# Performance work log

Measured on AMD Instinct MI355X. Metric: run time of the kernel, lower is better.

Reference implementation:

```python
import jax, jax.numpy as jnp
import numpy as np

B, S, E, D, H, L, V = 8, 128, 512, 1024, 16, 4, 32000
DH = D // H
FF = 4 * D
SCALE = 1.0 / (DH ** 0.5)
NEG = -1e30


def _layer_norm(x, g, b, eps=1e-5):
    m = jnp.mean(x, axis=-1, keepdims=True)
    v = jnp.mean((x - m) ** 2, axis=-1, keepdims=True)
    return (x - m) / jnp.sqrt(v + eps) * g + b


def _rel_shift(x):
    # x: [q, k, b, n] -> TransformerXL relative shift
    q, k, b, n = x.shape
    xp = jnp.concatenate([jnp.zeros((q, 1, b, n), x.dtype), x], axis=1)
    xp = xp.reshape(k + 1, q, b, n)
    return xp[1:].reshape(q, k, b, n)


def setup_inputs():
    key = jax.random.key(0)
    ks = jax.random.split(key, 40)
    g = lambda i, shape, s=0.02: jax.random.normal(ks[i], shape, jnp.float32) * s
    inp = {
        'input_ids': jax.random.randint(ks[0], (B, E), 0, V),
        'encoder_rep': jax.random.normal(ks[1], (B, E, D), jnp.float32),
        'input_mask': jnp.ones((B, E), jnp.float32),
        'decode_input': jax.random.randint(ks[2], (B, S), 0, V),
        'decode_target': jax.random.randint(ks[3], (B, S), 0, V),
        'word_emb': g(4, (V, D)),
        'qkv_w': g(5, (L, 3 * D, D)), 'r_w': g(6, (L, D, D)), 'o_w': g(7, (L, D, D)),
        'kv_w': g(8, (L, 2 * D, D)), 'q_w': g(9, (L, D, D)), 'io_w': g(10, (L, D, D)),
        'rr_bias': g(11, (L, H, DH)), 'rw_bias': g(12, (L, H, DH)),
        'ln1_g': jnp.ones((L, D)), 'ln1_b': jnp.zeros((L, D)),
        'ln2_g': jnp.ones((L, D)), 'ln2_b': jnp.zeros((L, D)),
        'ffn_w1': g(13, (L, FF, D)), 'ffn_b1': jnp.zeros((L, FF)),
        'ffn_w2': g(14, (L, D, FF)), 'ffn_b2': jnp.zeros((L, D)),
        'ln3_g': jnp.ones((L, D)), 'ln3_b': jnp.zeros((L, D)),
        'out_w': g(15, (D, D)), 'out_b': jnp.zeros((D,)),
        'copy_w': g(16, (D, D)), 'copy_b': jnp.zeros((D,)),
        'mode_w': g(17, (1, D)), 'mode_b': jnp.zeros((1,)),
    }
    return inp


def _forward(input_ids, encoder_rep, input_mask, decode_input, decode_target,
             word_emb, qkv_w, r_w, o_w, kv_w, q_w, io_w, rr_bias, rw_bias,
             ln1_g, ln1_b, ln2_g, ln2_b, ffn_w1, ffn_b1, ffn_w2, ffn_b2,
             ln3_g, ln3_b, out_w, out_b, copy_w, copy_b, mode_w, mode_b):
    # relative position embedding r: [S, D]
    pos_seq = jnp.arange(S - 1, -1, -1.0, dtype=jnp.float32)
    inv_freq = 1.0 / (10000.0 ** (jnp.arange(0.0, D, 2.0) / D))
    sin_inp = pos_seq[:, None] * inv_freq[None, :]
    r = jnp.concatenate([jnp.sin(sin_inp), jnp.cos(sin_inp)], axis=-1)

    causal = jnp.tril(jnp.ones((S, S), jnp.bool_))[:, :, None, None]  # [i,j,1,1]
    enc_mask_t = input_mask.T  # [E, B]

    core = word_emb[decode_input].transpose(1, 0, 2)  # [S, B, D]
    enc_t = encoder_rep.transpose(1, 0, 2)            # [E, B, D]

    for l in range(L):
        w = core
        heads = w @ qkv_w[l].T  # [S,B,3D]
        q, k, v = jnp.split(heads, 3, axis=-1)
        q = q.reshape(S, B, H, DH); k = k.reshape(S, B, H, DH); v = v.reshape(S, B, H, DH)
        r_k = (r @ r_w[l].T).reshape(S, H, DH)
        AC = jnp.einsum('ibnd,jbnd->ijbn', q + rw_bias[l], k)
        BD = _rel_shift(jnp.einsum('ibnd,jnd->ijbn', q + rr_bias[l], r_k))
        score = (AC + BD) * SCALE
        score = jnp.where(causal, score, NEG)
        prob = jax.nn.softmax(score, axis=1)
        vec = jnp.einsum('ijbn,jbnd->ibnd', prob, v).reshape(S, B, D)
        x = _layer_norm(w + vec @ o_w[l].T, ln1_g[l], ln1_b[l])

        # cross attention
        kv = enc_t @ kv_w[l].T
        k2, v2 = jnp.split(kv, 2, axis=-1)
        k2 = k2.reshape(E, B, H, DH); v2 = v2.reshape(E, B, H, DH)
        q2 = (x @ q_w[l].T).reshape(S, B, H, DH)
        score2 = jnp.einsum('qbnd,kbnd->qkbn', q2, k2) * SCALE
        score2 = score2 + (1.0 - enc_mask_t)[None, :, :, None] * NEG
        prob2 = jax.nn.softmax(score2, axis=1)
        vec2 = jnp.einsum('ijbn,jbnd->ibnd', prob2, v2).reshape(S, B, D)
        y = _layer_norm(x + vec2 @ io_w[l].T, ln2_g[l], ln2_b[l])

        # FFN (exact GELU as torch nn.GELU default)
        h = jax.nn.gelu(y @ ffn_w1[l].T + ffn_b1[l], approximate=False)
        h = h @ ffn_w2[l].T + ffn_b2[l]
        core = _layer_norm(y + h, ln3_g[l], ln3_b[l])

    core_out = core.transpose(1, 0, 2)  # [B, S, D]
    output = core_out @ out_w.T + out_b
    vocab_logits = output @ word_emb.T  # [B,S,V]
    vocab_prob = jax.nn.softmax(vocab_logits, axis=-1)

    copy_h = core_out @ copy_w.T + copy_b
    input_logits = jnp.einsum('bid,bjd->bij', copy_h, encoder_rep)
    input_logits = input_logits + (1.0 - input_mask[:, None, :]) * NEG
    input_prob = jax.nn.softmax(input_logits, axis=-1)  # [B,S,E]

    mode_sig = jax.nn.sigmoid(core_out @ mode_w.T + mode_b)  # [B,S,1]
    vocab_prob = vocab_prob * mode_sig

    idx = jnp.broadcast_to(input_ids[:, None, :], (B, S, E))
    b_i = jnp.arange(B)[:, None, None]
    s_i = jnp.arange(S)[None, :, None]
    vocab_prob = vocab_prob.at[b_i, s_i, idx].add((1.0 - mode_sig) * input_prob)

    flat = vocab_prob.reshape(-1, V)
    tgt = decode_target.reshape(-1)
    predict = jnp.take_along_axis(flat, tgt[:, None], axis=1)[:, 0]
    valid = (tgt != 0).astype(jnp.float32)
    loss = jnp.sum(-jnp.log(predict + 1e-6) * valid) / jnp.sum(valid)
    return jnp.repeat(loss[None], B)


def reference(input_ids, encoder_rep, input_mask, decode_input, decode_target,
              word_emb, qkv_w, r_w, o_w, kv_w, q_w, io_w, rr_bias, rw_bias,
              ln1_g, ln1_b, ln2_g, ln2_b, ffn_w1, ffn_b1, ffn_w2, ffn_b2,
              ln3_g, ln3_b, out_w, out_b, copy_w, copy_b, mode_w, mode_b):
    return _forward(input_ids, encoder_rep, input_mask, decode_input, decode_target,
                    word_emb, qkv_w, r_w, o_w, kv_w, q_w, io_w, rr_bias, rw_bias,
                    ln1_g, ln1_b, ln2_g, ln2_b, ffn_w1, ffn_b1, ffn_w2, ffn_b2,
                    ln3_g, ln3_b, out_w, out_b, copy_w, copy_b, mode_w, mode_b)
```

## Files before the change

kernel.cpp:

```cpp
#include <hip/hip_runtime.h>
#include <math.h>

#define B_ 8
#define S_ 128
#define E_ 512
#define D_ 1024
#define H_ 16
#define L_ 4
#define V_ 32000
#define DH_ 64
#define FF_ 4096
#define M_ 1024
#define ME_ 4096
#define NT_ 125
#define SCALE_F 0.125f
#define NEGV (-1e30f)

typedef __attribute__((ext_vector_type(8))) short short8;
typedef __attribute__((ext_vector_type(4))) float f32x4;

__device__ __forceinline__ float bf2f(ushort u) {
  union { unsigned int u32; float f; } v; v.u32 = ((unsigned int)u) << 16; return v.f;
}
__device__ __forceinline__ ushort f2bf(float x) {
  union { float f; unsigned int u; } v; v.f = x;
  unsigned int r = v.u + 0x7fff + ((v.u >> 16) & 1);
  return (ushort)(r >> 16);
}
__device__ __forceinline__ void gl_lds16(const ushort* g, ushort* l) {
  __builtin_amdgcn_global_load_lds((const __attribute__((address_space(1))) void*)g,
                                   (__attribute__((address_space(3))) void*)l, 16, 0, 0);
}

__device__ __forceinline__ float warp_reduce_sum(float v) {
#pragma unroll
  for (int o = 32; o > 0; o >>= 1) v += __shfl_down(v, o);
  return v;
}
__device__ __forceinline__ float warp_reduce_max(float v) {
#pragma unroll
  for (int o = 32; o > 0; o >>= 1) v = fmaxf(v, __shfl_down(v, o));
  return v;
}
__device__ __forceinline__ float block_reduce_sum(float v, float* sred) {
  v = warp_reduce_sum(v);
  __syncthreads();
  if ((threadIdx.x & 63) == 0) sred[threadIdx.x >> 6] = v;
  __syncthreads();
  float s = 0.0f;
  int nw = blockDim.x >> 6;
  for (int w = 0; w < nw; ++w) s += sred[w];
  return s;
}
__device__ __forceinline__ float block_reduce_max(float v, float* sred) {
  v = warp_reduce_max(v);
  __syncthreads();
  if ((threadIdx.x & 63) == 0) sred[threadIdx.x >> 6] = v;
  __syncthreads();
  float s = -3.4e38f;
  int nw = blockDim.x >> 6;
  for (int w = 0; w < nw; ++w) s = fmaxf(s, sred[w]);
  return s;
}

__global__ __launch_bounds__(256) void castf_kernel(const float* __restrict__ in,
                                                    ushort* __restrict__ out, int n4) {
  int t = blockIdx.x * 256 + threadIdx.x;
  if (t >= n4) return;
  float4 v = ((const float4*)in)[t];
  ushort4 o;
  o.x = f2bf(v.x); o.y = f2bf(v.y); o.z = f2bf(v.z); o.w = f2bf(v.w);
  ((ushort4*)out)[t] = o;
}

__global__ __launch_bounds__(256) void castlayer_kernel(
    const float* __restrict__ sqkv, const float* __restrict__ so,
    const float* __restrict__ sq, const float* __restrict__ sio,
    const float* __restrict__ sf1, const float* __restrict__ sf2,
    ushort* __restrict__ dqkv, ushort* __restrict__ dov,
    ushort* __restrict__ dq, ushort* __restrict__ dio,
    ushort* __restrict__ df1, ushort* __restrict__ df2) {
  int t = blockIdx.x * 256 + threadIdx.x;
  const float* src; ushort* dst; int idx;
  if (t < 786432)       { src = sqkv; dst = dqkv; idx = t; }
  else if (t < 1048576) { src = so;  dst = dov; idx = t - 786432; }
  else if (t < 1310720) { src = sq;  dst = dq;  idx = t - 1048576; }
  else if (t < 1572864) { src = sio; dst = dio; idx = t - 1310720; }
  else if (t < 2621440) { src = sf1; dst = df1; idx = t - 1572864; }
  else if (t < 3670016) { src = sf2; dst = df2; idx = t - 2621440; }
  else return;
  float4 v = ((const float4*)src)[idx];
  ushort4 o4;
  o4.x = f2bf(v.x); o4.y = f2bf(v.y); o4.z = f2bf(v.z); o4.w = f2bf(v.w);
  ((ushort4*)dst)[idx] = o4;
}

__global__ __launch_bounds__(256) void enc_both_kernel(const float* __restrict__ enc,
                                                       ushort* __restrict__ enc_bf,
                                                       ushort* __restrict__ encT) {
  int t = blockIdx.x * 256 + threadIdx.x;
  if (t >= ME_ * D_) return;
  ushort bv = f2bf(enc[t]);
  enc_bf[t] = bv;
  int d = t & (D_ - 1);
  int be = t >> 10;
  int b = be >> 9, e = be & (E_ - 1);
  encT[((size_t)(e * B_ + b) << 10) + d] = bv;
}

__global__ __launch_bounds__(256) void pos_emb_kernel(ushort* __restrict__ r) {
  int t = blockIdx.x * 256 + threadIdx.x;
  if (t >= S_ * D_) return;
  int i = t / D_, j = t % D_;
  float pos = (float)(S_ - 1 - i);
  int jj = (j < D_ / 2) ? j : (j - D_ / 2);
  float invf = powf(10000.0f, -(float)(2 * jj) / (float)D_);
  float a = pos * invf;
  r[t] = f2bf((j < D_ / 2) ? sinf(a) : cosf(a));
}

__global__ __launch_bounds__(256) void embed_kernel(const int* __restrict__ ids,
                                                    const float* __restrict__ emb,
                                                    float* __restrict__ core,
                                                    ushort* __restrict__ core_bf) {
  int t = blockIdx.x * 256 + threadIdx.x;
  if (t >= M_ * D_) return;
  int d = t & (D_ - 1);
  int row = t >> 10;
  int s = row >> 3, b = row & 7;
  float v = emb[(size_t)ids[b * S_ + s] * D_ + d];
  core[t] = v;
  core_bf[t] = f2bf(v);
}

template <int EPI>
__global__ __launch_bounds__(256) void gemm_w_kernel(
    const ushort* __restrict__ A, const ushort* __restrict__ Bm,
    const float* __restrict__ bias, void* __restrict__ Cv,
    int M, int N, int K, int ksplit,
    long long Arow, long long Abatch, long long Brow, long long Bbatch,
    long long Crow, long long Cbatch, long long Csplit) {
  __shared__ ushort lA[128 * 32];
  __shared__ ushort lB[128 * 32];
  int tid = threadIdx.x;
  int bz = blockIdx.z;
  int batch = bz / ksplit, split = bz % ksplit;
  int kLen = K / ksplit, kStart = split * kLen;
  const ushort* Ab = A + (size_t)batch * Abatch;
  const ushort* Bb = Bm + (size_t)batch * Bbatch;
  int bm = blockIdx.y * 128, bn = blockIdx.x * 128;
  int lane = tid & 63, wave = tid >> 6;
  int wrow = (wave >> 1) * 64, wcol = (wave & 1) * 64;
  int quad = lane >> 4, l16 = lane & 15;
  f32x4 acc[4][4];
#pragma unroll
  for (int i = 0; i < 4; ++i)
#pragma unroll
    for (int j = 0; j < 4; ++j) { acc[i][j][0] = 0.f; acc[i][j][1] = 0.f; acc[i][j][2] = 0.f; acc[i][j][3] = 0.f; }
  int r0 = tid >> 2, c0 = (tid & 3) * 8;
  int r1 = (tid + 256) >> 2;
  for (int k0 = kStart; k0 < kStart + kLen; k0 += 32) {
    __syncthreads();
    gl_lds16(Ab + (size_t)(bm + r0) * Arow + k0 + c0, &lA[(size_t)tid * 8]);
    gl_lds16(Ab + (size_t)(bm + r1) * Arow + k0 + c0, &lA[(size_t)(256 + tid) * 8]);
    gl_lds16(Bb + (size_t)(bn + r0) * Brow + k0 + c0, &lB[(size_t)tid * 8]);
    gl_lds16(Bb + (size_t)(bn + r1) * Brow + k0 + c0, &lB[(size_t)(256 + tid) * 8]);
    __syncthreads();
    short8 af[4], bfr[4];
#pragma unroll
    for (int mi = 0; mi < 4; ++mi)
      af[mi] = *(const short8*)&lA[(size_t)(wrow + mi * 16 + l16) * 32 + quad * 8];
#pragma unroll
    for (int ni = 0; ni < 4; ++ni)
      bfr[ni] = *(const short8*)&lB[(size_t)(wcol + ni * 16 + l16) * 32 + quad * 8];
#pragma unroll
    for (int mi = 0; mi < 4; ++mi)
#pragma unroll
      for (int ni = 0; ni < 4; ++ni)
        acc[mi][ni] = __builtin_amdgcn_mfma_f32_16x16x32_bf16(af[mi], bfr[ni], acc[mi][ni], 0, 0, 0);
  }
#pragma unroll
  for (int mi = 0; mi < 4; ++mi) {
    int row0 = bm + wrow + mi * 16 + quad * 4;
#pragma unroll
    for (int ni = 0; ni < 4; ++ni) {
      int col = bn + wcol + ni * 16 + l16;
      float bv = 0.f;
      if (EPI >= 3) bv = bias[col];
#pragma unroll
      for (int r = 0; r < 4; ++r) {
        float v = acc[mi][ni][r] + bv;
        if (EPI == 4) v = 0.5f * v * (1.0f + erff(v * 0.70710678118654752f));
        size_t ci = (size_t)split * Csplit + (size_t)batch * Cbatch + (size_t)(row0 + r) * Crow + col;
        if (EPI == 0) ((float*)Cv)[ci] = v;
        else ((ushort*)Cv)[ci] = f2bf(v);
      }
    }
  }
}

template <int EPI>
__global__ __launch_bounds__(512, 2) void gemm256_kernel(
    const ushort* __restrict__ A, const ushort* __restrict__ Bm, void* __restrict__ Cv,
    float* __restrict__ tmax, float* __restrict__ tsum,
    long long Arow, long long Abatch, long long Brow, long long Bbatch,
    long long Crow, long long Cbatch) {
  __shared__ ushort sT[4][2][2][128 * 32];
  __shared__ float smax[256][4];
  __shared__ float ssum[256][4];
  const int NK = 32;
  int tid = threadIdx.x;
  int bm, bn, bnT = 0, batch = 0;
  if constexpr (EPI == 5) {
    int orig = blockIdx.x;
    int xcd = orig & 7;
    int base = (xcd < 4) ? xcd * 63 : 4 * 63 + (xcd - 4) * 62;
    int wg = base + (orig >> 3);
    bm = (wg & 3) * 256;
    bnT = wg >> 2;
    bn = bnT * 256;
  } else {
    bn = blockIdx.x * 256;
    bm = blockIdx.y * 256;
    batch = blockIdx.z;
  }
  const ushort* Ab = A + (size_t)batch * Abatch;
  const ushort* Bb = Bm + (size_t)batch * Bbatch;
  int lane = tid & 63, wave = tid >> 6;
  int wr = wave >> 2;
  int wc = wave & 3;
  int bhalf = wc >> 1;
  int brow0 = (wc & 1) * 64;
  int quad = lane >> 4, l16 = lane & 15;
  int sr = tid >> 2;
  int sslot = (((tid & 3) ^ ((sr >> 1) & 3)) * 8);
  int rsw = (quad ^ ((l16 >> 1) & 3)) * 8;

  f32x4 acc[8][4];
#pragma unroll
  for (int i = 0; i < 8; ++i)
#pragma unroll
    for (int j = 0; j < 4; ++j) { acc[i][j][0]=0.f; acc[i][j][1]=0.f; acc[i][j][2]=0.f; acc[i][j][3]=0.f; }

#define STAGE_HALF(s_, ab_, h_)                                                        \
  do {                                                                                 \
    int s__ = (s_); int b__ = s__ & 3;                                                 \
    if ((ab_) == 0)                                                                    \
      gl_lds16(Ab + (size_t)(bm + (h_) * 128 + sr) * Arow + s__ * 32 + sslot,          \
               &sT[b__][0][h_][tid * 8]);                                              \
    else                                                                               \
      gl_lds16(Bb + (size_t)(bn + (h_) * 128 + sr) * Brow + s__ * 32 + sslot,          \
               &sT[b__][1][h_][tid * 8]);                                              \
  } while (0)

#pragma unroll
  for (int s = 0; s < 3; ++s) {
    STAGE_HALF(s, 0, 0); STAGE_HALF(s, 0, 1);
    STAGE_HALF(s, 1, 0); STAGE_HALF(s, 1, 1);
  }
  asm volatile("s_waitcnt vmcnt(8)");
  __builtin_amdgcn_s_barrier();
  __builtin_amdgcn_sched_barrier(0);

  short8 af[4], bfv[4];
  for (int t = 0; t < NK; ++t) {
    int bt = t & 3;
#pragma unroll
    for (int i = 0; i < 4; ++i)
      af[i] = *(const short8*)&sT[bt][0][wr][(i * 16 + l16) * 32 + rsw];
#pragma unroll
    for (int i = 0; i < 4; ++i)
      bfv[i] = *(const short8*)&sT[bt][1][bhalf][(brow0 + i * 16 + l16) * 32 + rsw];
    if (t + 3 < NK) { STAGE_HALF(t + 3, 0, 0); STAGE_HALF(t + 3, 0, 1); }
    __builtin_amdgcn_s_barrier();
    __builtin_amdgcn_sched_barrier(0);
    __builtin_amdgcn_s_setprio(1);
#pragma unroll
    for (int mi = 0; mi < 4; ++mi)
#pragma unroll
      for (int ni = 0; ni < 4; ++ni)
        acc[mi][ni] = __builtin_amdgcn_mfma_f32_16x16x32_bf16(af[mi], bfv[ni], acc[mi][ni], 0, 0, 0);
    __builtin_amdgcn_s_setprio(0);
    __builtin_amdgcn_s_barrier();
    __builtin_amdgcn_sched_barrier(0);
#pragma unroll
    for (int i = 0; i < 4; ++i)
      af[i] = *(const short8*)&sT[bt][0][wr][((4 + i) * 16 + l16) * 32 + rsw];
    if (t + 3 < NK) { STAGE_HALF(t + 3, 1, 0); STAGE_HALF(t + 3, 1, 1); }
    if (t + 3 < NK)      asm volatile("s_waitcnt vmcnt(8)");
    else if (t + 2 < NK) asm volatile("s_waitcnt vmcnt(4)");
    else                 asm volatile("s_waitcnt vmcnt(0)");
    __builtin_amdgcn_s_barrier();
    __builtin_amdgcn_sched_barrier(0);
    __builtin_amdgcn_s_setprio(1);
#pragma unroll
    for (int mi = 0; mi < 4; ++mi)
#pragma unroll
      for (int ni = 0; ni < 4; ++ni)
        acc[4 + mi][ni] = __builtin_amdgcn_mfma_f32_16x16x32_bf16(af[mi], bfv[ni], acc[4 + mi][ni], 0, 0, 0);
    __builtin_amdgcn_s_setprio(0);
    __builtin_amdgcn_s_barrier();
    __builtin_amdgcn_sched_barrier(0);
  }
#undef STAGE_HALF

  if constexpr (EPI == 5) {
#pragma unroll
    for (int mi = 0; mi < 8; ++mi)
#pragma unroll
      for (int r = 0; r < 4; ++r) {
        int rr = wr * 128 + mi * 16 + quad * 4 + r;
        float lm = -3.4e38f;
#pragma unroll
        for (int ni = 0; ni < 4; ++ni) lm = fmaxf(lm, acc[mi][ni][r]);
#pragma unroll
        for (int o = 1; o < 16; o <<= 1) lm = fmaxf(lm, __shfl_xor(lm, o));
        if (l16 == 0) smax[rr][wc] = lm;
      }
    __syncthreads();
#pragma unroll
    for (int mi = 0; mi < 8; ++mi)
#pragma unroll
      for (int r = 0; r < 4; ++r) {
        int rr = wr * 128 + mi * 16 + quad * 4 + r;
        float m = fmaxf(fmaxf(smax[rr][0], smax[rr][1]), fmaxf(smax[rr][2], smax[rr][3]));
        float ls = 0.f;
#pragma unroll
        for (int ni = 0; ni < 4; ++ni) ls += __expf(acc[mi][ni][r] - m);
#pragma unroll
        for (int o = 1; o < 16; o <<= 1) ls += __shfl_xor(ls, o);
        if (l16 == 0) ssum[rr][wc] = ls;
      }
    __syncthreads();
    if (tid < 256) {
      float m = fmaxf(fmaxf(smax[tid][0], smax[tid][1]), fmaxf(smax[tid][2], smax[tid][3]));
      float s = ssum[tid][0] + ssum[tid][1] + ssum[tid][2] + ssum[tid][3];
      tmax[(size_t)(bm + tid) * NT_ + bnT] = m;
      tsum[(size_t)(bm + tid) * NT_ + bnT] = s;
    }
  } else {
    ushort* C = (ushort*)Cv + (size_t)batch * Cbatch;
#pragma unroll
    for (int mi = 0; mi < 8; ++mi) {
      int row0 = bm + wr * 128 + mi * 16 + quad * 4;
#pragma unroll
      for (int ni = 0; ni < 4; ++ni) {
        int col = bn + wc * 64 + ni * 16 + l16;
#pragma unroll
        for (int r = 0; r < 4; ++r)
          C[(size_t)(row0 + r) * Crow + col] = f2bf(acc[mi][ni][r]);
      }
    }
  }
}

__global__ __launch_bounds__(256) void vocab_combine_kernel(const float* __restrict__ tmax,
                                                            const float* __restrict__ tsum,
                                                            const ushort* __restrict__ headout,
                                                            const ushort* __restrict__ emb,
                                                            const int* __restrict__ tgt,
                                                            float* __restrict__ rmax,
                                                            float* __restrict__ rsum,
                                                            float* __restrict__ tl) {
  __shared__ float sred[4];
  int m = blockIdx.x;
  float mx = -3.4e38f;
  for (int t = threadIdx.x; t < NT_; t += 256) mx = fmaxf(mx, tmax[(size_t)m * NT_ + t]);
  mx = block_reduce_max(mx, sred);
  float s = 0.f;
  for (int t = threadIdx.x; t < NT_; t += 256)
    s += tsum[(size_t)m * NT_ + t] * expf(tmax[(size_t)m * NT_ + t] - mx);
  s = block_reduce_sum(s, sred);
  int si = m >> 3, b = m & 7;
  int t = tgt[b * S_ + si];
  const ushort* a = headout + (size_t)m * 2048;
  const ushort* w = emb + (size_t)t * D_;
  float acc = 0.f;
  for (int i = threadIdx.x; i < D_; i += 256) acc += bf2f(a[i]) * bf2f(w[i]);
  acc = block_reduce_sum(acc, sred);
  if (threadIdx.x == 0) { rmax[m] = mx; rsum[m] = s; tl[m] = acc; }
}

__global__ __launch_bounds__(256) void attn1_fused_kernel(const ushort* __restrict__ heads,
                                                          const ushort* __restrict__ rkproj,
                                                          const float* __restrict__ rw,
                                                          const float* __restrict__ rr,
                                                          ushort* __restrict__ attnA) {
  __shared__ float score[128][129];
  __shared__ ushort pP[128][136];
  __shared__ ushort vT[64][136];
  int bz = blockIdx.x;
  int b = bz >> 4, n = bz & 15;
  int tid = threadIdx.x, lane = tid & 63, wave = tid >> 6;
  int quad = lane >> 4, l16 = lane & 15;
  int wrow = wave * 32;

  {
    int j = tid >> 1, dbase = (tid & 1) * 32;
    const ushort* src = heads + (size_t)(j * 8 + b) * 3072 + 2048 + n * 64 + dbase;
#pragma unroll
    for (int c8 = 0; c8 < 4; ++c8) {
      short8 v8 = *(const short8*)(src + c8 * 8);
#pragma unroll
      for (int cc = 0; cc < 8; ++cc) vT[dbase + c8 * 8 + cc][j] = (ushort)v8[cc];
    }
  }

  short8 qrw[2][2], qrr[2][2];
#pragma unroll
  for (int mi = 0; mi < 2; ++mi) {
    int i = wrow + mi * 16 + l16;
    const ushort* qp = heads + (size_t)(i * 8 + b) * 3072 + n * 64;
#pragma unroll
    for (int kc = 0; kc < 2; ++kc) {
      int k0 = kc * 32 + quad * 8;
      short8 qv = *(const short8*)(qp + k0);
      short8 w, rv;
#pragma unroll
      for (int t = 0; t < 8; ++t) {
        float q = bf2f((ushort)qv[t]);
        w[t] = (short)f2bf(q + rw[n * 64 + k0 + t]);
        rv[t] = (short)f2bf(q + rr[n * 64 + k0 + t]);
      }
      qrw[mi][kc] = w; qrr[mi][kc] = rv;
    }
  }

  {
    f32x4 acc[2][8];
#pragma unroll
    for (int i = 0; i < 2; ++i)
#pragma unroll
      for (int j = 0; j < 8; ++j) { acc[i][j][0]=0.f; acc[i][j][1]=0.f; acc[i][j][2]=0.f; acc[i][j][3]=0.f; }
#pragma unroll
    for (int kc = 0; kc < 2; ++kc) {
      int k0 = kc * 32 + quad * 8;
      short8 kf[8];
#pragma unroll
      for (int ni = 0; ni < 8; ++ni) {
        int j = ni * 16 + l16;
        kf[ni] = *(const short8*)(heads + (size_t)(j * 8 + b) * 3072 + 1024 + n * 64 + k0);
      }
#pragma unroll
      for (int mi = 0; mi < 2; ++mi)
#pragma unroll
        for (int ni = 0; ni < 8; ++ni)
          acc[mi][ni] = __builtin_amdgcn_mfma_f32_16x16x32_bf16(qrw[mi][kc], kf[ni], acc[mi][ni], 0, 0, 0);
    }
#pragma unroll
    for (int mi = 0; mi < 2; ++mi)
#pragma unroll
      for (int ni = 0; ni < 8; ++ni)
#pragma unroll
        for (int r = 0; r < 4; ++r)
          score[wrow + mi * 16 + quad * 4 + r][ni * 16 + l16] = acc[mi][ni][r];
  }
  {
    f32x4 acc[2][8];
#pragma unroll
    for (int i = 0; i < 2; ++i)
#pragma unroll
      for (int j = 0; j < 8; ++j) { acc[i][j][0]=0.f; acc[i][j][1]=0.f; acc[i][j][2]=0.f; acc[i][j][3]=0.f; }
#pragma unroll
    for (int kc = 0; kc < 2; ++kc) {
      int k0 = kc * 32 + quad * 8;
      short8 rkf[8];
#pragma unroll
      for (int ni = 0; ni < 8; ++ni) {
        int jp = ni * 16 + l16;
        rkf[ni] = *(const short8*)(rkproj + (size_t)jp * 1024 + n * 64 + k0);
      }
#pragma unroll
      for (int mi = 0; mi < 2; ++mi)
#pragma unroll
        for (int ni = 0; ni < 8; ++ni)
          acc[mi][ni] = __builtin_amdgcn_mfma_f32_16x16x32_bf16(qrr[mi][kc], rkf[ni], acc[mi][ni], 0, 0, 0);
    }
#pragma unroll
    for (int mi = 0; mi < 2; ++mi)
#pragma unroll
      for (int r = 0; r < 4; ++r) {
        int i = wrow + mi * 16 + quad * 4 + r;
#pragma unroll
        for (int ni = 0; ni < 8; ++ni) {
          int jp = ni * 16 + l16;
          if (jp >= 127 - i) score[i][jp - 127 + i] += acc[mi][ni][r];
        }
      }
  }
  {
    int row = tid >> 1, halfc = (tid & 1) * 64;
    float mx = -3.4e38f;
    for (int c = halfc; c < halfc + 64; ++c) {
      float v = (c <= row) ? score[row][c] * SCALE_F : -3.4e38f;
      mx = fmaxf(mx, v);
    }
    mx = fmaxf(mx, __shfl_xor(mx, 1));
    float s = 0.f;
    for (int c = halfc; c < halfc + 64; ++c) {
      float e = (c <= row) ? __expf(score[row][c] * SCALE_F - mx) : 0.f;
      score[row][c] = e;
      s += e;
    }
    s += __shfl_xor(s, 1);
    float inv = 1.0f / s;
    for (int c = halfc; c < halfc + 64; ++c) pP[row][c] = f2bf(score[row][c] * inv);
  }
  __syncthreads();
  {
    f32x4 acc[2][4];
#pragma unroll
    for (int i = 0; i < 2; ++i)
#pragma unroll
      for (int j = 0; j < 4; ++j) { acc[i][j][0]=0.f; acc[i][j][1]=0.f; acc[i][j][2]=0.f; acc[i][j][3]=0.f; }
#pragma unroll
    for (int kc = 0; kc < 4; ++kc) {
      int k0 = kc * 32 + quad * 8;
      short8 pf[2], vf[4];
#pragma unroll
      for (int mi = 0; mi < 2; ++mi)
        pf[mi] = *(const short8*)&pP[wrow + mi * 16 + l16][k0];
#pragma unroll
      for (int ni = 0; ni < 4; ++ni)
        vf[ni] = *(const short8*)&vT[ni * 16 + l16][k0];
#pragma unroll
      for (int mi = 0; mi < 2; ++mi)
#pragma unroll
        for (int ni = 0; ni < 4; ++ni)
          acc[mi][ni] = __builtin_amdgcn_mfma_f32_16x16x32_bf16(pf[mi], vf[ni], acc[mi][ni], 0, 0, 0);
    }
#pragma unroll
    for (int mi = 0; mi < 2; ++mi)
#pragma unroll
      for (int r = 0; r < 4; ++r) {
        int i = wrow + mi * 16 + quad * 4 + r;
#pragma unroll
        for (int ni = 0; ni < 4; ++ni)
          attnA[(size_t)(i * 8 + b) * 1024 + n * 64 + ni * 16 + l16] = f2bf(acc[mi][ni][r]);
      }
  }
}

__global__ __launch_bounds__(256) void attn2_fused_kernel(const float* __restrict__ q0,
                                                          const float* __restrict__ q1,
                                                          const ushort* __restrict__ kvproj,
                                                          const float* __restrict__ mask,
                                                          ushort* __restrict__ attnA) {
  __shared__ ushort vT[64][136];
  __shared__ ushort pP[128][136];
  __shared__ float mtile[128];
  int bz = blockIdx.x;
  int b = bz >> 4, n = bz & 15;
  int tid = threadIdx.x, lane = tid & 63, wave = tid >> 6;
  int quad = lane >> 4, l16 = lane & 15;
  int wrow = wave * 32;
  short8 qf[2][2];
#pragma unroll
  for (int mi = 0; mi < 2; ++mi) {
    int i = wrow + mi * 16 + l16;
    size_t base = (size_t)(i * 8 + b) * 1024 + n * 64;
#pragma unroll
    for (int kc = 0; kc < 2; ++kc) {
      int k0 = kc * 32 + quad * 8;
      short8 v;
#pragma unroll
      for (int t = 0; t < 8; ++t) v[t] = (short)f2bf(q0[base + k0 + t] + q1[base + k0 + t]);
      qf[mi][kc] = v;
    }
  }
  float m_run[2][4], l_run[2][4];
#pragma unroll
  for (int mi = 0; mi < 2; ++mi)
#pragma unroll
    for (int r = 0; r < 4; ++r) { m_run[mi][r] = -3.0e38f; l_run[mi][r] = 0.f; }
  f32x4 accO[2][4];
#pragma unroll
  for (int i = 0; i < 2; ++i)
#pragma unroll
    for (int j = 0; j < 4; ++j) { accO[i][j][0]=0.f; accO[i][j][1]=0.f; accO[i][j][2]=0.f; accO[i][j][3]=0.f; }

  for (int et = 0; et < 4; ++et) {
    __syncthreads();
    {
      int j = tid >> 1, dbase = (tid & 1) * 32;
      int e = et * 128 + j;
      const ushort* src = kvproj + (size_t)(e * 8 + b) * 2048 + 1024 + n * 64 + dbase;
#pragma unroll
      for (int c8 = 0; c8 < 4; ++c8) {
        short8 v8 = *(const short8*)(src + c8 * 8);
#pragma unroll
        for (int cc = 0; cc < 8; ++cc) vT[dbase + c8 * 8 + cc][j] = (ushort)v8[cc];
      }
      if (tid < 128) mtile[tid] = (1.0f - mask[b * E_ + et * 128 + tid]) * NEGV;
    }
    f32x4 accS[2][8];
#pragma unroll
    for (int i = 0; i < 2; ++i)
#pragma unroll
      for (int j = 0; j < 8; ++j) { accS[i][j][0]=0.f; accS[i][j][1]=0.f; accS[i][j][2]=0.f; accS[i][j][3]=0.f; }
#pragma unroll
    for (int kc = 0; kc < 2; ++kc) {
      int k0 = kc * 32 + quad * 8;
      short8 kf[8];
#pragma unroll
      for (int ni = 0; ni < 8; ++ni) {
        int e = et * 128 + ni * 16 + l16;
        kf[ni] = *(const short8*)(kvproj + (size_t)(e * 8 + b) * 2048 + n * 64 + k0);
      }
#pragma unroll
      for (int mi = 0; mi < 2; ++mi)
#pragma unroll
        for (int ni = 0; ni < 8; ++ni)
          accS[mi][ni] = __builtin_amdgcn_mfma_f32_16x16x32_bf16(qf[mi][kc], kf[ni], accS[mi][ni], 0, 0, 0);
    }
    __syncthreads();
#pragma unroll
    for (int mi = 0; mi < 2; ++mi)
#pragma unroll
      for (int r = 0; r < 4; ++r) {
        float v[8];
        float vmax = -3.4e38f;
#pragma unroll
        for (int ni = 0; ni < 8; ++ni) {
          v[ni] = accS[mi][ni][r] * SCALE_F + mtile[ni * 16 + l16];
          vmax = fmaxf(vmax, v[ni]);
        }
#pragma unroll
        for (int o = 1; o < 16; o <<= 1) vmax = fmaxf(vmax, __shfl_xor(vmax, o));
        float mnew = fmaxf(m_run[mi][r], vmax);
        float alpha = __expf(m_run[mi][r] - mnew);
        float ls = 0.f;
        int row = wrow + mi * 16 + quad * 4 + r;
#pragma unroll
        for (int ni = 0; ni < 8; ++ni) {
          float p = __expf(v[ni] - mnew);
          ls += p;
          pP[row][ni * 16 + l16] = f2bf(p);
        }
#pragma unroll
        for (int o = 1; o < 16; o <<= 1) ls += __shfl_xor(ls, o);
        l_run[mi][r] = l_run[mi][r] * alpha + ls;
        m_run[mi][r] = mnew;
#pragma unroll
        for (int ni = 0; ni < 4; ++ni) accO[mi][ni][r] *= alpha;
      }
#pragma unroll
    for (int kc = 0; kc < 4; ++kc) {
      int k0 = kc * 32 + quad * 8;
      short8 pf[2], vf[4];
#pragma unroll
      for (int mi = 0; mi < 2; ++mi)
        pf[mi] = *(const short8*)&pP[wrow + mi * 16 + l16][k0];
#pragma unroll
      for (int ni = 0; ni < 4; ++ni)
        vf[ni] = *(const short8*)&vT[ni * 16 + l16][k0];
#pragma unroll
      for (int mi = 0; mi < 2; ++mi)
#pragma unroll
        for (int ni = 0; ni < 4; ++ni)
          accO[mi][ni] = __builtin_amdgcn_mfma_f32_16x16x32_bf16(pf[mi], vf[ni], accO[mi][ni], 0, 0, 0);
    }
  }
#pragma unroll
  for (int mi = 0; mi < 2; ++mi)
#pragma unroll
    for (int r = 0; r < 4; ++r) {
      int i = wrow + mi * 16 + quad * 4 + r;
      float inv = 1.0f / l_run[mi][r];
#pragma unroll
      for (int ni = 0; ni < 4; ++ni)
        attnA[(size_t)(i * 8 + b) * 1024 + n * 64 + ni * 16 + l16] = f2bf(accO[mi][ni][r] * inv);
    }
}

__global__ __launch_bounds__(256) void addln_kernel(const float* __restrict__ a,
                                                    const float* __restrict__ c,
                                                    int nsplit, long long cstride,
                                                    const float* __restrict__ bias,
                                                    const float* __restrict__ g,
                                                    const float* __restrict__ bb,
                                                    float* __restrict__ out,
                                                    ushort* __restrict__ out_bf,
                                                    const float* __restrict__ mw,
                                                    const float* __restrict__ mb,
                                                    float* __restrict__ msig) {
  __shared__ float sred[4];
  int row = blockIdx.x;
  const float* pa = a + (size_t)row * D_;
  float vals[4];
  float s = 0.f;
#pragma unroll
  for (int it = 0; it < 4; ++it) {
    int idx = threadIdx.x + it * 256;
    float v = pa[idx];
    for (int sp = 0; sp < nsplit; ++sp) v += c[(size_t)sp * cstride + (size_t)row * D_ + idx];
    if (bias) v += bias[idx];
    vals[it] = v;
    s += v;
  }
  s = block_reduce_sum(s, sred);
  float mean = s * (1.0f / D_);
  float ss = 0.f;
#pragma unroll
  for (int it = 0; it < 4; ++it) {
    float dd = vals[it] - mean;
    ss += dd * dd;
  }
  ss = block_reduce_sum(ss, sred);
  float inv = rsqrtf(ss * (1.0f / D_) + 1e-5f);
#pragma unroll
  for (int it = 0; it < 4; ++it) {
    int idx = threadIdx.x + it * 256;
    float r = (vals[it] - mean) * inv * g[idx] + bb[idx];
    vals[it] = r;
    out[(size_t)row * D_ + idx] = r;
    out_bf[(size_t)row * D_ + idx] = f2bf(r);
  }
  if (mw) {
    float sm = 0.f;
#pragma unroll
    for (int it = 0; it < 4; ++it) {
      int idx = threadIdx.x + it * 256;
      sm += vals[it] * mw[idx];
    }
    sm = block_reduce_sum(sm, sred);
    if (threadIdx.x == 0) msig[row] = 1.0f / (1.0f + expf(-(sm + mb[0])));
  }
}

__global__ __launch_bounds__(256) void final_kernel(const float* __restrict__ lg,
                                                    const int* __restrict__ ids,
                                                    const float* __restrict__ mask,
                                                    const int* __restrict__ tgt,
                                                    const float* __restrict__ mode_sig,
                                                    const float* __restrict__ tlogit,
                                                    const float* __restrict__ rmax,
                                                    const float* __restrict__ rsum,
                                                    float* __restrict__ loss_acc) {
  __shared__ float sred[4];
  int s = blockIdx.x, b = blockIdx.y;
  int m = s * B_ + b;
  size_t base = (size_t)(b * S_ + s) * E_;
  const long long LGS = (long long)B_ * S_ * E_;
  int tg = tgt[b * S_ + s];
  float lv[2];
  float mx = -3.4e38f;
#pragma unroll
  for (int it = 0; it < 2; ++it) {
    int e = threadIdx.x + it * 256;
    float raw = 0.f;
#pragma unroll
    for (int sp = 0; sp < 4; ++sp) raw += lg[sp * LGS + base + e];
    raw += (1.0f - mask[b * E_ + e]) * NEGV;
    lv[it] = raw;
    mx = fmaxf(mx, raw);
  }
  mx = block_reduce_max(mx, sred);
  float ssum = 0.f, csum = 0.f;
#pragma unroll
  for (int it = 0; it < 2; ++it) {
    int e = threadIdx.x + it * 256;
    float ev = expf(lv[it] - mx);
    ssum += ev;
    if (ids[b * E_ + e] == tg) csum += ev;
  }
  ssum = block_reduce_sum(ssum, sred);
  csum = block_reduce_sum(csum, sred);
  if (threadIdx.x == 0) {
    float copy_p = csum / ssum;
    float pv = expf(tlogit[m] - rmax[m]) / rsum[m];
    float msig = mode_sig[m];
    float predict = pv * msig + (1.0f - msig) * copy_p;
    float valid = (tg != 0) ? 1.0f : 0.0f;
    atomicAdd(&loss_acc[0], -logf(predict + 1e-6f) * valid);
    atomicAdd(&loss_acc[1], valid);
  }
}

__global__ void writeout_kernel(const float* __restrict__ loss_acc, float* __restrict__ out) {
  if (threadIdx.x < B_) out[threadIdx.x] = loss_acc[0] / loss_acc[1];
}

static void gw(hipStream_t st, int epi, const ushort* A, const ushort* B, const float* bias,
               void* C, int M, int N, int K,
               long long Ar, long long Ab, long long Br, long long Bb,
               long long Cr, long long Cb, int nb, int ksplit, long long Csplit) {
  dim3 g(N / 128, M / 128, nb * ksplit);
  switch (epi) {
    case 0: gemm_w_kernel<0><<<g, 256, 0, st>>>(A, B, bias, C, M, N, K, ksplit, Ar, Ab, Br, Bb, Cr, Cb, Csplit); break;
    case 1: gemm_w_kernel<1><<<g, 256, 0, st>>>(A, B, bias, C, M, N, K, ksplit, Ar, Ab, Br, Bb, Cr, Cb, Csplit); break;
    case 3: gemm_w_kernel<3><<<g, 256, 0, st>>>(A, B, bias, C, M, N, K, ksplit, Ar, Ab, Br, Bb, Cr, Cb, Csplit); break;
    case 4: gemm_w_kernel<4><<<g, 256, 0, st>>>(A, B, bias, C, M, N, K, ksplit, Ar, Ab, Br, Bb, Cr, Cb, Csplit); break;
  }
}
static void castTo(hipStream_t st, const float* src, ushort* dst, size_t count) {
  int n4 = (int)(count / 4);
  castf_kernel<<<(n4 + 255) / 256, 256, 0, st>>>(src, dst, n4);
}

extern "C" void kernel_launch(void* const* d_in, const int* in_sizes, int n_in,
                              void* d_out, int out_size, void* d_ws, size_t ws_size,
                              hipStream_t stream) {
  const int* input_ids = (const int*)d_in[0];
  const float* encoder_rep = (const float*)d_in[1];
  const float* input_mask = (const float*)d_in[2];
  const int* decode_input = (const int*)d_in[3];
  const int* decode_target = (const int*)d_in[4];
  const float* word_emb = (const float*)d_in[5];
  const float* qkv_w = (const float*)d_in[6];
  const float* r_w = (const float*)d_in[7];
  const float* o_w = (const float*)d_in[8];
  const float* kv_w = (const float*)d_in[9];
  const float* q_w = (const float*)d_in[10];
  const float* io_w = (const float*)d_in[11];
  const float* rr_bias = (const float*)d_in[12];
  const float* rw_bias = (const float*)d_in[13];
  const float* ln1_g = (const float*)d_in[14];
  const float* ln1_b = (const float*)d_in[15];
  const float* ln2_g = (const float*)d_in[16];
  const float* ln2_b = (const float*)d_in[17];
  const float* ffn_w1 = (const float*)d_in[18];
  const float* ffn_b1 = (const float*)d_in[19];
  const float* ffn_w2 = (const float*)d_in[20];
  const float* ffn_b2 = (const float*)d_in[21];
  const float* ln3_g = (const float*)d_in[22];
  const float* ln3_b = (const float*)d_in[23];
  const float* out_w = (const float*)d_in[24];
  const float* out_b = (const float*)d_in[25];
  const float* copy_w = (const float*)d_in[26];
  const float* copy_b = (const float*)d_in[27];
  const float* mode_w = (const float*)d_in[28];
  const float* mode_b = (const float*)d_in[29];
  float* out = (float*)d_out;

  char* base = (char*)d_ws;
  size_t off = 0;
  auto alloc = [&](size_t bytes) -> void* {
    void* p = base + off;
    off = (off + bytes + 255) & ~(size_t)255;
    return p;
  };

  ushort* wl_qkv = (ushort*)alloc((size_t)3 * D_ * D_ * 2);
  ushort* wl_o = (ushort*)alloc((size_t)D_ * D_ * 2);
  ushort* wl_q = (ushort*)alloc((size_t)D_ * D_ * 2);
  ushort* wl_io = (ushort*)alloc((size_t)D_ * D_ * 2);
  ushort* wl_f1 = (ushort*)alloc((size_t)FF_ * D_ * 2);
  ushort* wl_f2 = (ushort*)alloc((size_t)FF_ * D_ * 2);
  ushort* wl_kv = (ushort*)alloc((size_t)L_ * 2 * D_ * D_ * 2);
  ushort* wl_r = (ushort*)alloc((size_t)L_ * D_ * D_ * 2);
  ushort* kvproj_bf = (ushort*)alloc((size_t)L_ * ME_ * 2 * D_ * 2);
  ushort* rkproj_bf = (ushort*)alloc((size_t)L_ * S_ * D_ * 2);

  ushort* w_emb = (ushort*)alloc((size_t)V_ * D_ * 2);
  ushort* w_oc = (ushort*)alloc((size_t)2048 * D_ * 2);
  float* b_oc = (float*)alloc(2048 * 4);
  ushort* enc_bf = (ushort*)alloc((size_t)ME_ * D_ * 2);
  ushort* encT_bf = (ushort*)alloc((size_t)ME_ * D_ * 2);
  ushort* r_bf = (ushort*)alloc((size_t)S_ * D_ * 2);
  float* f_core = (float*)alloc((size_t)M_ * D_ * 4);
  ushort* core_bf = (ushort*)alloc((size_t)M_ * D_ * 2);
  ushort* heads_bf = (ushort*)alloc((size_t)M_ * 3 * D_ * 2);
  ushort* attnA_bf = (ushort*)alloc((size_t)M_ * D_ * 2);
  float* f_tmp = (float*)alloc((size_t)4 * M_ * D_ * 4);
  float* f_x = (float*)alloc((size_t)M_ * D_ * 4);
  ushort* x_bf = (ushort*)alloc((size_t)M_ * D_ * 2);
  float* f_y = (float*)alloc((size_t)M_ * D_ * 4);
  ushort* y_bf = (ushort*)alloc((size_t)M_ * D_ * 2);
  float* f_q = (float*)alloc((size_t)2 * M_ * D_ * 4);
  ushort* ffnh_bf = (ushort*)alloc((size_t)M_ * FF_ * 2);
  ushort* headout_bf = (ushort*)alloc((size_t)M_ * 2048 * 2);
  float* f_lg = (float*)alloc((size_t)4 * B_ * S_ * E_ * 4);
  float* f_tmax = (float*)alloc((size_t)M_ * NT_ * 4);
  float* f_tsum = (float*)alloc((size_t)M_ * NT_ * 4);
  float* f_rmax = (float*)alloc(M_ * 4);
  float* f_rsum = (float*)alloc(M_ * 4);
  float* f_tlogit = (float*)alloc(M_ * 4);
  float* f_mode = (float*)alloc(M_ * 4);
  float* f_loss = (float*)alloc(64);

  castTo(stream, word_emb, w_emb, (size_t)V_ * D_);
  castTo(stream, out_w, w_oc, (size_t)D_ * D_);
  castTo(stream, copy_w, w_oc + (size_t)D_ * D_, (size_t)D_ * D_);
  hipMemcpyAsync(b_oc, out_b, D_ * 4, hipMemcpyDeviceToDevice, stream);
  hipMemcpyAsync(b_oc + D_, copy_b, D_ * 4, hipMemcpyDeviceToDevice, stream);
  enc_both_kernel<<<(ME_ * D_) / 256, 256, 0, stream>>>(encoder_rep, enc_bf, encT_bf);
  pos_emb_kernel<<<(S_ * D_ + 255) / 256, 256, 0, stream>>>(r_bf);
  embed_kernel<<<(M_ * D_) / 256, 256, 0, stream>>>(decode_input, word_emb, f_core, core_bf);

  castTo(stream, kv_w, wl_kv, (size_t)L_ * 2 * D_ * D_);
  castTo(stream, r_w, wl_r, (size_t)L_ * D_ * D_);
  gemm256_kernel<1><<<dim3(2 * D_ / 256, ME_ / 256, L_), 512, 0, stream>>>(
      encT_bf, wl_kv, kvproj_bf, nullptr, nullptr,
      D_, 0, D_, (long long)2 * D_ * D_, 2 * D_, (long long)ME_ * 2 * D_);
  gw(stream, 1, r_bf, wl_r, nullptr, rkproj_bf, S_, D_, D_,
     D_, 0, D_, (long long)D_ * D_, D_, (long long)S_ * D_, L_, 1, 0);

  for (int l = 0; l < L_; ++l) {
    castlayer_kernel<<<14336, 256, 0, stream>>>(
        qkv_w + (size_t)l * 3 * D_ * D_, o_w + (size_t)l * D_ * D_,
        q_w + (size_t)l * D_ * D_, io_w + (size_t)l * D_ * D_,
        ffn_w1 + (size_t)l * FF_ * D_, ffn_w2 + (size_t)l * FF_ * D_,
        wl_qkv, wl_o, wl_q, wl_io, wl_f1, wl_f2);

    gw(stream, 1, core_bf, wl_qkv, nullptr, heads_bf, M_, 3 * D_, D_, D_, 0, D_, 0, 3 * D_, 0, 1, 1, 0);
    attn1_fused_kernel<<<B_ * H_, 256, 0, stream>>>(heads_bf, rkproj_bf + (size_t)l * S_ * D_,
                                                    rw_bias + (size_t)l * D_,
                                                    rr_bias + (size_t)l * D_, attnA_bf);
    gw(stream, 0, attnA_bf, wl_o, nullptr, f_tmp, M_, D_, D_, D_, 0, D_, 0, D_, 0, 1, 2,
       (long long)M_ * D_);
    addln_kernel<<<M_, 256, 0, stream>>>(f_core, f_tmp, 2, (long long)M_ * D_, nullptr,
                                         ln1_g + (size_t)l * D_, ln1_b + (size_t)l * D_, f_x, x_bf,
                                         nullptr, nullptr, nullptr);

    gw(stream, 0, x_bf, wl_q, nullptr, f_q, M_, D_, D_, D_, 0, D_, 0, D_, 0, 1, 2,
       (long long)M_ * D_);
    attn2_fused_kernel<<<B_ * H_, 256, 0, stream>>>(f_q, f_q + (size_t)M_ * D_,
                                                    kvproj_bf + (size_t)l * ME_ * 2 * D_,
                                                    input_mask, attnA_bf);
    gw(stream, 0, attnA_bf, wl_io, nullptr, f_tmp, M_, D_, D_, D_, 0, D_, 0, D_, 0, 1, 2,
       (long long)M_ * D_);
    addln_kernel<<<M_, 256, 0, stream>>>(f_x, f_tmp, 2, (long long)M_ * D_, nullptr,
                                         ln2_g + (size_t)l * D_, ln2_b + (size_t)l * D_, f_y, y_bf,
                                         nullptr, nullptr, nullptr);

    gw(stream, 4, y_bf, wl_f1, ffn_b1 + (size_t)l * FF_, ffnh_bf, M_, FF_, D_, D_, 0, D_, 0, FF_, 0, 1, 1, 0);
    gw(stream, 0, ffnh_bf, wl_f2, nullptr, f_tmp, M_, D_, FF_, FF_, 0, FF_, 0, D_, 0, 1, 4,
       (long long)M_ * D_);
    bool last = (l == L_ - 1);
    addln_kernel<<<M_, 256, 0, stream>>>(f_y, f_tmp, 4, (long long)M_ * D_,
                                         ffn_b2 + (size_t)l * D_,
                                         ln3_g + (size_t)l * D_, ln3_b + (size_t)l * D_, f_core, core_bf,
                                         last ? mode_w : nullptr, last ? mode_b : nullptr,
                                         last ? f_mode : nullptr);
  }

  gw(stream, 3, core_bf, w_oc, b_oc, headout_bf, M_, 2048, D_, D_, 0, D_, 0, 2048, 0, 1, 1, 0);

  gemm256_kernel<5><<<500, 512, 0, stream>>>(headout_bf, w_emb, nullptr, f_tmax, f_tsum,
                                             2048, 0, D_, 0, 0, 0);
  vocab_combine_kernel<<<M_, 256, 0, stream>>>(f_tmax, f_tsum, headout_bf, w_emb, decode_target,
                                               f_rmax, f_rsum, f_tlogit);

  gw(stream, 0, headout_bf + D_, enc_bf, nullptr, f_lg, S_, E_, D_,
     (long long)B_ * 2048, 2048, D_, (long long)E_ * D_, E_, (long long)S_ * E_, B_, 4,
     (long long)B_ * S_ * E_);

  hipMemsetAsync(f_loss, 0, 2 * sizeof(float), stream);
  final_kernel<<<dim3(S_, B_), 256, 0, stream>>>(f_lg, input_ids, input_mask, decode_target,
                                                 f_mode, f_tlogit, f_rmax, f_rsum, f_loss);
  writeout_kernel<<<1, 64, 0, stream>>>(f_loss, out);
}
```

Before: 1.573 ms.

## Simplify 256x256 GEMM pipeline to double-buffered LDS with single MFMA phase

Reduces the LDS ring in the 256-tile GEMM from four stages to two and issues a full K-tile of A and B loads at once, two tiles ahead. Each iteration now loads all eight A fragments and runs one 32-MFMA block with one barrier pair, replacing two interleaved half-phases. This halves LDS use (possibly better occupancy) and cuts barriers. In exchange, prefetch depth drops and more registers hold A fragments, which may expose global-load latency.

```diff
diff --git a/kernel.cpp b/kernel.cpp
--- a/kernel.cpp
+++ b/kernel.cpp
@@ -205,7 +205,7 @@
     float* __restrict__ tmax, float* __restrict__ tsum,
     long long Arow, long long Abatch, long long Brow, long long Bbatch,
     long long Crow, long long Cbatch) {
-  __shared__ ushort sT[4][2][2][128 * 32];
+  __shared__ ushort sT[2][2][2][128 * 32];
   __shared__ float smax[256][4];
   __shared__ float ssum[256][4];
   const int NK = 32;
@@ -242,67 +242,53 @@
 #pragma unroll
     for (int j = 0; j < 4; ++j) { acc[i][j][0]=0.f; acc[i][j][1]=0.f; acc[i][j][2]=0.f; acc[i][j][3]=0.f; }
 
-#define STAGE_HALF(s_, ab_, h_)                                                        \
+#define STAGE_TILE(s_)                                                                 \
   do {                                                                                 \
-    int s__ = (s_); int b__ = s__ & 3;                                                 \
-    if ((ab_) == 0)                                                                    \
-      gl_lds16(Ab + (size_t)(bm + (h_) * 128 + sr) * Arow + s__ * 32 + sslot,          \
-               &sT[b__][0][h_][tid * 8]);                                              \
-    else                                                                               \
-      gl_lds16(Bb + (size_t)(bn + (h_) * 128 + sr) * Brow + s__ * 32 + sslot,          \
-               &sT[b__][1][h_][tid * 8]);                                              \
+    int s__ = (s_); int b__ = s__ & 1;                                                 \
+    gl_lds16(Ab + (size_t)(bm + sr) * Arow + s__ * 32 + sslot,                         \
+             &sT[b__][0][0][tid * 8]);                                                 \
+    gl_lds16(Ab + (size_t)(bm + 128 + sr) * Arow + s__ * 32 + sslot,                   \
+             &sT[b__][0][1][tid * 8]);                                                 \
+    gl_lds16(Bb + (size_t)(bn + sr) * Brow + s__ * 32 + sslot,                         \
+             &sT[b__][1][0][tid * 8]);                                                 \
+    gl_lds16(Bb + (size_t)(bn + 128 + sr) * Brow + s__ * 32 + sslot,                   \
+             &sT[b__][1][1][tid * 8]);                                                 \
   } while (0)
 
-#pragma unroll
-  for (int s = 0; s < 3; ++s) {
-    STAGE_HALF(s, 0, 0); STAGE_HALF(s, 0, 1);
-    STAGE_HALF(s, 1, 0); STAGE_HALF(s, 1, 1);
-  }
-  asm volatile("s_waitcnt vmcnt(8)");
+  STAGE_TILE(0);
+  STAGE_TILE(1);
+  asm volatile("s_waitcnt vmcnt(4)" ::: "memory");
   __builtin_amdgcn_s_barrier();
   __builtin_amdgcn_sched_barrier(0);
 
-  short8 af[4], bfv[4];
   for (int t = 0; t < NK; ++t) {
-    int bt = t & 3;
-#pragma unroll
-    for (int i = 0; i < 4; ++i)
+    int bt = t & 1;
+    short8 af[8], bfv[4];
+#pragma unroll
+    for (int i = 0; i < 8; ++i)
       af[i] = *(const short8*)&sT[bt][0][wr][(i * 16 + l16) * 32 + rsw];
 #pragma unroll
     for (int i = 0; i < 4; ++i)
       bfv[i] = *(const short8*)&sT[bt][1][bhalf][(brow0 + i * 16 + l16) * 32 + rsw];
-    if (t + 3 < NK) { STAGE_HALF(t + 3, 0, 0); STAGE_HALF(t + 3, 0, 1); }
-    __builtin_amdgcn_s_barrier();
-    __builtin_amdgcn_sched_barrier(0);
     __builtin_amdgcn_s_setprio(1);
 #pragma unroll
-    for (int mi = 0; mi < 4; ++mi)
+    for (int mi = 0; mi < 8; ++mi)
 #pragma unroll
       for (int ni = 0; ni < 4; ++ni)
         acc[mi][ni] = __builtin_amdgcn_mfma_f32_16x16x32_bf16(af[mi], bfv[ni], acc[mi][ni], 0, 0, 0);
     __builtin_amdgcn_s_setprio(0);
     __builtin_amdgcn_s_barrier();
     __builtin_amdgcn_sched_barrier(0);
-#pragma unroll
-    for (int i = 0; i < 4; ++i)
-      af[i] = *(const short8*)&sT[bt][0][wr][((4 + i) * 16 + l16) * 32 + rsw];
-    if (t + 3 < NK) { STAGE_HALF(t + 3, 1, 0); STAGE_HALF(t + 3, 1, 1); }
-    if (t + 3 < NK)      asm volatile("s_waitcnt vmcnt(8)");
-    else if (t + 2 < NK) asm volatile("s_waitcnt vmcnt(4)");
-    else                 asm volatile("s_waitcnt vmcnt(0)");
+    if (t + 2 < NK) {
+      STAGE_TILE(t + 2);
+      asm volatile("s_waitcnt vmcnt(4)" ::: "memory");
+    } else {
+      asm volatile("s_waitcnt vmcnt(0)" ::: "memory");
+    }
     __builtin_amdgcn_s_barrier();
     __builtin_amdgcn_sched_barrier(0);
-    __builtin_amdgcn_s_setprio(1);
-#pragma unroll
-    for (int mi = 0; mi < 4; ++mi)
-#pragma unroll
-      for (int ni = 0; ni < 4; ++ni)
-        acc[4 + mi][ni] = __builtin_amdgcn_mfma_f32_16x16x32_bf16(af[mi], bfv[ni], acc[4 + mi][ni], 0, 0, 0);
-    __builtin_amdgcn_s_setprio(0);
-    __builtin_amdgcn_s_barrier();
-    __builtin_amdgcn_sched_barrier(0);
-  }
-#undef STAGE_HALF
+  }
+#undef STAGE_TILE
 
   if constexpr (EPI == 5) {
 #pragma unroll
```

New measurement: 1.583 ms. About the same (+0.6%).
